# Optimization experiments

Hardware: AMD Instinct MI355X
Metric: run time of the kernel (lower is better)

Reference implementation:

```python
import jax, jax.numpy as jnp
import numpy as np

DIM = 1024
HEADS = 16
DIM_HEAD = 64
INNER = HEADS * DIM_HEAD
SCALE = DIM_HEAD ** -0.5


def setup_inputs() -> dict:
    key = jax.random.key(0)
    kx, kq, kk, kv, ko = jax.random.split(key, 5)
    B, N = 2, 2048
    s = DIM ** -0.5
    return {
        "x": jax.random.normal(kx, (B, N, DIM), dtype=jnp.float32),
        "Wq": jax.random.normal(kq, (DIM, INNER), dtype=jnp.float32) * s,
        "Wk": jax.random.normal(kk, (DIM, INNER), dtype=jnp.float32) * s,
        "Wv": jax.random.normal(kv, (DIM, INNER), dtype=jnp.float32) * s,
        "Wo": jax.random.normal(ko, (INNER, DIM), dtype=jnp.float32) * s,
    }


def reference(x, Wq, Wk, Wv, Wo):
    B, N, _ = x.shape
    # projections, split heads: b n (h d) -> b h n d
    def split(t):
        return t.reshape(B, N, HEADS, DIM_HEAD).transpose(0, 2, 1, 3)
    q = split(x @ Wq)
    k = split(x @ Wk)
    v = split(x @ Wv)
    # scores [B,H,N,N]
    dots = jnp.einsum("bhnd,bhmd->bhnm", q, k) * SCALE
    # causal mask: positions j > i masked
    causal = jnp.triu(jnp.ones((N, N), dtype=bool), k=1)
    dots = jnp.where(causal, -jnp.inf, dots)
    attn = jax.nn.softmax(dots, axis=-1)
    out = jnp.einsum("bhnm,bhmd->bhnd", attn, v)
    out = out.transpose(0, 2, 1, 3).reshape(B, N, INNER)
    return out @ Wo
```

## Files before the change

### kernel.cpp

```cpp
#include <hip/hip_runtime.h>

typedef unsigned short u16;
typedef unsigned int u32;
typedef __attribute__((ext_vector_type(8))) short short8;
typedef __attribute__((ext_vector_type(4))) short s16x4;
typedef __attribute__((ext_vector_type(4))) float f32x4;
typedef __attribute__((ext_vector_type(16))) float f32x16;
typedef __attribute__((ext_vector_type(4))) u32 u32x4;

typedef const __attribute__((address_space(1))) void* gptr_t;
typedef __attribute__((address_space(3))) void* sptr_t;

#define N_SEQ 2048
#define DIM 1024
#define INNER 1024
#define NTOK 4096
#define QKV_LD 3072

__device__ __forceinline__ u16 f2b(float f) {
  union { float f; unsigned u; } v; v.f = f;
  unsigned r = v.u + 0x7fffu + ((v.u >> 16) & 1u);
  return (u16)(r >> 16);
}

__global__ __launch_bounds__(256) void cast_x_kernel(const float* __restrict__ src,
                                                     u16* __restrict__ dst) {
  const size_t i = (size_t)blockIdx.x * 256 + threadIdx.x;
  const f32x4* s = (const f32x4*)(src + i * 8);
  f32x4 a = s[0], b = s[1];
  short8 o;
#pragma unroll
  for (int j = 0; j < 4; ++j) { o[j] = (short)f2b(a[j]); o[4 + j] = (short)f2b(b[j]); }
  *(short8*)(dst + i * 8) = o;
}

__global__ __launch_bounds__(256) void transpose_cast4_kernel(const float* __restrict__ Wq,
                                                              const float* __restrict__ Wk,
                                                              const float* __restrict__ Wv,
                                                              const float* __restrict__ Wo,
                                                              u16* __restrict__ wqkvt,
                                                              u16* __restrict__ wot) {
  const int z = blockIdx.z;
  const float* src = (z == 0) ? Wq : (z == 1) ? Wk : (z == 2) ? Wv : Wo;
  u16* dst = (z == 3) ? wot : wqkvt + (size_t)z * 1024 * 1024;
  __shared__ u16 tile[64][65];
  const int n0 = blockIdx.x * 64, k0 = blockIdx.y * 64;
  for (int i = threadIdx.x; i < 4096; i += 256) {
    const int r = i >> 6, c = i & 63;
    tile[r][c] = f2b(src[(size_t)(k0 + r) * 1024 + n0 + c]);
  }
  __syncthreads();
  for (int i = threadIdx.x; i < 4096; i += 256) {
    const int r = i >> 6, c = i & 63;
    dst[(size_t)(n0 + r) * 1024 + k0 + c] = tile[c][r];
  }
}

__global__ __launch_bounds__(256) void transpose_v_kernel(const u16* __restrict__ qkv,
                                                          u16* __restrict__ vt) {
  __shared__ u16 t[64][72];
  const int nt0 = blockIdx.x * 64;
  const int bh = blockIdx.y;
  const int b = bh >> 4, h = bh & 15;
  const u16* src = qkv + (size_t)b * N_SEQ * QKV_LD + 2048 + h * 64;
#pragma unroll
  for (int i = 0; i < 2; ++i) {
    const int cid = i * 256 + threadIdx.x;
    const int r = cid >> 3, c = (cid & 7) * 8;
    *(short8*)&t[r][c] = *(const short8*)(src + (size_t)(nt0 + r) * QKV_LD + c);
  }
  __syncthreads();
#pragma unroll
  for (int i = 0; i < 2; ++i) {
    const int cid = i * 256 + threadIdx.x;
    const int d = cid >> 3, c = (cid & 7) * 8;
    short8 v;
#pragma unroll
    for (int j = 0; j < 8; ++j) v[j] = t[c + j][d];
    *(short8*)(vt + ((size_t)bh * 64 + d) * N_SEQ + nt0 + c) = v;
  }
}

template <typename OutT>
__global__ __launch_bounds__(256) void gemm_tn(const u16* __restrict__ A,
                                               const u16* __restrict__ Bt,
                                               OutT* __restrict__ C,
                                               int M, int N, int K) {
  __shared__ u16 Al[128 * 64];
  __shared__ u16 Bl[128 * 64];
  const int tid = threadIdx.x;
  const int w = tid >> 6, lane = tid & 63;
  const int l15 = lane & 15, lg = lane >> 4;
  const int wr = w >> 1, wc = w & 1;
  const int nwg = gridDim.x * gridDim.y;
  int bid = blockIdx.y * gridDim.x + blockIdx.x;
  bid = (bid & 7) * (nwg >> 3) + (bid >> 3);
  const int bx = bid % gridDim.x, by = bid / gridDim.x;
  const int m0 = by * 128, n0 = bx * 128;

  f32x4 acc[4][4] = {};

  for (int k0 = 0; k0 < K; k0 += 64) {
#pragma unroll
    for (int i = 0; i < 4; ++i) {
      const int chunk = (w << 2) + i;
      const int e = (chunk << 9) + lane * 8;
      const int row = e >> 6, col = e & 63;
      const u16* ga = A + (size_t)(m0 + row) * K + k0 + col;
      __builtin_amdgcn_global_load_lds((gptr_t)ga, (sptr_t)(Al + (chunk << 9)), 16, 0, 0);
      const u16* gb = Bt + (size_t)(n0 + row) * K + k0 + col;
      __builtin_amdgcn_global_load_lds((gptr_t)gb, (sptr_t)(Bl + (chunk << 9)), 16, 0, 0);
    }
    __syncthreads();
#pragma unroll
    for (int kk = 0; kk < 2; ++kk) {
      short8 af[4], bf[4];
#pragma unroll
      for (int m = 0; m < 4; ++m)
        af[m] = *(const short8*)(Al + ((wr * 64 + m * 16 + l15) << 6) + kk * 32 + lg * 8);
#pragma unroll
      for (int n = 0; n < 4; ++n)
        bf[n] = *(const short8*)(Bl + ((wc * 64 + n * 16 + l15) << 6) + kk * 32 + lg * 8);
#pragma unroll
      for (int m = 0; m < 4; ++m)
#pragma unroll
        for (int n = 0; n < 4; ++n)
          acc[m][n] = __builtin_amdgcn_mfma_f32_16x16x32_bf16(af[m], bf[n], acc[m][n], 0, 0, 0);
    }
    __syncthreads();
  }

#pragma unroll
  for (int m = 0; m < 4; ++m)
#pragma unroll
    for (int n = 0; n < 4; ++n)
#pragma unroll
      for (int r = 0; r < 4; ++r) {
        const int row = m0 + wr * 64 + m * 16 + lg * 4 + r;
        const int col = n0 + wc * 64 + n * 16 + l15;
        const float v = acc[m][n][r];
        if constexpr (sizeof(OutT) == 2) C[(size_t)row * N + col] = (OutT)f2b(v);
        else                             C[(size_t)row * N + col] = (OutT)v;
      }
}

__global__ __launch_bounds__(64) void attn_kernel(const u16* __restrict__ qkv,
                                                  const u16* __restrict__ vt,
                                                  u16* __restrict__ attnb) {
  const int bx = blockIdx.x;
  const int bh = bx & 31;
  const int qw = 63 - (bx >> 5);
  const int b = bh >> 4, h = bh & 15;
  const int lane = threadIdx.x;
  const int l31 = lane & 31, hh = lane >> 5;
  const int qrow = qw * 32 + l31;

  __shared__ u16 Kl[64 * 64];
  __shared__ u16 Vl[64 * 64];

  const u16* base  = qkv + (size_t)b * N_SEQ * QKV_LD;
  const u16* kbase = base + 1024 + h * 64;
  const u16* vbase = vt + (size_t)bh * 64 * N_SEQ;

  short8 bq[4];
#pragma unroll
  for (int ks = 0; ks < 4; ++ks)
    bq[ks] = *(const short8*)(base + (size_t)qrow * QKV_LD + h * 64 + ks * 16 + hh * 8);

  f32x16 o0 = {}, o1 = {};
  float m_run = -3.0e38f, l_run = 0.f;
  const float kscale = 0.125f * 1.4426950408889634f;
  const int nt = (qw >> 1) + 1;

  for (int jt = 0; jt < nt; ++jt) {
    const int kvs = jt * 64;

#pragma unroll
    for (int i = 0; i < 8; ++i) {
      const int cid = i * 64 + lane;
      const int row = cid >> 3, cs = (cid & 7) ^ (row & 7);
      __builtin_amdgcn_global_load_lds(
          (gptr_t)(kbase + (size_t)(kvs + row) * QKV_LD + cs * 8),
          (sptr_t)(Kl + i * 512), 16, 0, 0);
      __builtin_amdgcn_global_load_lds(
          (gptr_t)(vbase + (size_t)row * N_SEQ + kvs + cs * 8),
          (sptr_t)(Vl + i * 512), 16, 0, 0);
    }
    asm volatile("s_waitcnt vmcnt(0)" ::: "memory");

    f32x16 p0 = {}, p1 = {};
    __builtin_amdgcn_s_setprio(1);
#pragma unroll
    for (int ks = 0; ks < 4; ++ks) {
      const int r0 = l31, r1 = 32 + l31;
      short8 ak0 = *(const short8*)(Kl + r0 * 64 + (((ks * 2 + hh) ^ (r0 & 7)) * 8));
      short8 ak1 = *(const short8*)(Kl + r1 * 64 + (((ks * 2 + hh) ^ (r1 & 7)) * 8));
      p0 = __builtin_amdgcn_mfma_f32_32x32x16_bf16(ak0, bq[ks], p0, 0, 0, 0);
      p1 = __builtin_amdgcn_mfma_f32_32x32x16_bf16(ak1, bq[ks], p1, 0, 0, 0);
    }
    __builtin_amdgcn_s_setprio(0);

    if (jt == nt - 1) {
      const int kvb = kvs + 4 * hh;
#pragma unroll
      for (int r = 0; r < 16; ++r) {
        const int off = (r & 3) + 8 * (r >> 2);
        if (kvb + off > qrow)      p0[r] = -3.0e38f;
        if (kvb + 32 + off > qrow) p1[r] = -3.0e38f;
      }
    }

    float mt = -3.0e38f;
#pragma unroll
    for (int r = 0; r < 16; ++r) { mt = fmaxf(mt, p0[r]); mt = fmaxf(mt, p1[r]); }
    mt = fmaxf(mt, __shfl_xor(mt, 32, 64));
    const float mn = fmaxf(m_run, mt);
    if (!__all(mn - m_run <= 44.f)) {
      const float sf = exp2f((m_run - mn) * kscale);
      m_run = mn;
      l_run *= sf;
      o0 *= sf; o1 *= sf;
    }
    float ps = 0.f;
#pragma unroll
    for (int r = 0; r < 16; ++r) {
      const float e0 = exp2f((p0[r] - m_run) * kscale);
      const float e1 = exp2f((p1[r] - m_run) * kscale);
      p0[r] = e0; p1[r] = e1;
      ps += e0 + e1;
    }
    ps += __shfl_xor(ps, 32, 64);
    l_run += ps;

    u32 bpw[4][4];
#define PACK_TILE(P, kf)                                                    \
    {                                                                       \
      _Pragma("unroll")                                                     \
      for (int a2 = 0; a2 < 2; ++a2) {                                      \
        _Pragma("unroll")                                                   \
        for (int c2 = 0; c2 < 2; ++c2) {                                    \
          u32 X, Y;                                                         \
          asm("v_cvt_pk_bf16_f32 %0, %1, %2" : "=v"(X)                      \
              : "v"(P[8 * a2 + 2 * c2]), "v"(P[8 * a2 + 2 * c2 + 1]));      \
          asm("v_cvt_pk_bf16_f32 %0, %1, %2" : "=v"(Y)                      \
              : "v"(P[8 * a2 + 4 + 2 * c2]), "v"(P[8 * a2 + 5 + 2 * c2]));  \
          asm("v_permlane32_swap_b32 %0, %1" : "+v"(X), "+v"(Y));           \
          bpw[(kf) * 2 + a2][c2] = X;                                       \
          bpw[(kf) * 2 + a2][2 + c2] = Y;                                   \
        }                                                                   \
      }                                                                     \
    }
    PACK_TILE(p0, 0)
    PACK_TILE(p1, 1)
#undef PACK_TILE

    __builtin_amdgcn_s_setprio(1);
#pragma unroll
    for (int ks16 = 0; ks16 < 4; ++ks16) {
      u32x4 t = {bpw[ks16][0], bpw[ks16][1], bpw[ks16][2], bpw[ks16][3]};
      short8 bp = __builtin_bit_cast(short8, t);
      const int cb = ks16 * 2 + hh;
      const int row0 = l31, row1 = 32 + l31;
      short8 av0 = *(const short8*)(Vl + row0 * 64 + ((cb ^ (row0 & 7)) * 8));
      short8 av1 = *(const short8*)(Vl + row1 * 64 + ((cb ^ (row1 & 7)) * 8));
      o0 = __builtin_amdgcn_mfma_f32_32x32x16_bf16(av0, bp, o0, 0, 0, 0);
      o1 = __builtin_amdgcn_mfma_f32_32x32x16_bf16(av1, bp, o1, 0, 0, 0);
    }
    __builtin_amdgcn_s_setprio(0);
  }

  const float inv = 1.f / l_run;
  u16* orow = attnb + ((size_t)b * N_SEQ + qrow) * INNER + h * 64 + 4 * hh;
#pragma unroll
  for (int rq = 0; rq < 4; ++rq) {
    s16x4 sv0, sv1;
#pragma unroll
    for (int j = 0; j < 4; ++j) {
      sv0[j] = (short)f2b(o0[rq * 4 + j] * inv);
      sv1[j] = (short)f2b(o1[rq * 4 + j] * inv);
    }
    *(s16x4*)(orow + rq * 8) = sv0;
    *(s16x4*)(orow + 32 + rq * 8) = sv1;
  }
}

extern "C" void kernel_launch(void* const* d_in, const int* in_sizes, int n_in,
                              void* d_out, int out_size, void* d_ws, size_t ws_size,
                              hipStream_t stream) {
  const float* x  = (const float*)d_in[0];
  const float* Wq = (const float*)d_in[1];
  const float* Wk = (const float*)d_in[2];
  const float* Wv = (const float*)d_in[3];
  const float* Wo = (const float*)d_in[4];
  float* out = (float*)d_out;

  u16* xb    = (u16*)d_ws;
  u16* wqkvt = xb    + (size_t)NTOK * DIM;
  u16* wot   = wqkvt + (size_t)3 * INNER * DIM;
  u16* qkv   = wot   + (size_t)DIM * INNER;
  u16* attnb = qkv   + (size_t)NTOK * QKV_LD;
  u16* vtb   = attnb + (size_t)NTOK * INNER;

  cast_x_kernel<<<dim3(NTOK * DIM / (256 * 8)), 256, 0, stream>>>(x, xb);
  transpose_cast4_kernel<<<dim3(16, 16, 4), 256, 0, stream>>>(Wq, Wk, Wv, Wo, wqkvt, wot);

  gemm_tn<u16><<<dim3(3072 / 128, 4096 / 128), 256, 0, stream>>>(xb, wqkvt, qkv, NTOK, 3072, DIM);
  transpose_v_kernel<<<dim3(32, 32), 256, 0, stream>>>(qkv, vtb);
  attn_kernel<<<dim3(2048), 64, 0, stream>>>(qkv, vtb, attnb);
  gemm_tn<float><<<dim3(1024 / 128, 4096 / 128), 256, 0, stream>>>(attnb, wot, out, NTOK, INNER, INNER);
}
```

Before: 160.4 us.

## Double-buffer K/V tiles in LDS and prioritize long-running attention waves

Splits the K/V LDS staging into two buffers so the next tile's global-to-LDS loads are issued before computing on the current tile, waiting only on the older batch of loads. Replaces per-MFMA-section priority toggling with a fixed high priority for waves handling the last query blocks, which have the most KV tiles. Also splits the softmax row-sum into four independent accumulators to shorten the dependency chain. This doubles LDS use per block, which could lower occupancy. Each wave reads only its own lanes' loads, so no barrier is needed with 64-thread blocks.

```diff
diff --git a/kernel.cpp b/kernel.cpp
--- a/kernel.cpp
+++ b/kernel.cpp
@@ -155,8 +155,10 @@
   const int l31 = lane & 31, hh = lane >> 5;
   const int qrow = qw * 32 + l31;
 
-  __shared__ u16 Kl[64 * 64];
-  __shared__ u16 Vl[64 * 64];
+  __shared__ u16 Kl[2][64 * 64];
+  __shared__ u16 Vl[2][64 * 64];
+
+  if (qw >= 48) __builtin_amdgcn_s_setprio(1);
 
   const u16* base  = qkv + (size_t)b * N_SEQ * QKV_LD;
   const u16* kbase = base + 1024 + h * 64;
@@ -172,33 +174,47 @@
   const float kscale = 0.125f * 1.4426950408889634f;
   const int nt = (qw >> 1) + 1;
 
+#define STAGE(jt_, bsel)                                                            \
+  {                                                                                 \
+    const int kvs_ = (jt_) * 64;                                                    \
+    u16* Klb_ = Kl[bsel];                                                           \
+    u16* Vlb_ = Vl[bsel];                                                           \
+    _Pragma("unroll")                                                               \
+    for (int i = 0; i < 8; ++i) {                                                   \
+      const int cid = i * 64 + lane;                                                \
+      const int row = cid >> 3, cs = (cid & 7) ^ (row & 7);                         \
+      __builtin_amdgcn_global_load_lds(                                             \
+          (gptr_t)(kbase + (size_t)(kvs_ + row) * QKV_LD + cs * 8),                 \
+          (sptr_t)(Klb_ + i * 512), 16, 0, 0);                                      \
+      __builtin_amdgcn_global_load_lds(                                             \
+          (gptr_t)(vbase + (size_t)row * N_SEQ + kvs_ + cs * 8),                    \
+          (sptr_t)(Vlb_ + i * 512), 16, 0, 0);                                      \
+    }                                                                               \
+  }
+
+  STAGE(0, 0)
+
   for (int jt = 0; jt < nt; ++jt) {
     const int kvs = jt * 64;
-
-#pragma unroll
-    for (int i = 0; i < 8; ++i) {
-      const int cid = i * 64 + lane;
-      const int row = cid >> 3, cs = (cid & 7) ^ (row & 7);
-      __builtin_amdgcn_global_load_lds(
-          (gptr_t)(kbase + (size_t)(kvs + row) * QKV_LD + cs * 8),
-          (sptr_t)(Kl + i * 512), 16, 0, 0);
-      __builtin_amdgcn_global_load_lds(
-          (gptr_t)(vbase + (size_t)row * N_SEQ + kvs + cs * 8),
-          (sptr_t)(Vl + i * 512), 16, 0, 0);
-    }
-    asm volatile("s_waitcnt vmcnt(0)" ::: "memory");
+    const int cur = jt & 1;
+    if (jt + 1 < nt) {
+      STAGE(jt + 1, cur ^ 1)
+      asm volatile("s_waitcnt vmcnt(16)" ::: "memory");
+    } else {
+      asm volatile("s_waitcnt vmcnt(0)" ::: "memory");
+    }
+    const u16* Klb = Kl[cur];
+    const u16* Vlb = Vl[cur];
 
     f32x16 p0 = {}, p1 = {};
-    __builtin_amdgcn_s_setprio(1);
 #pragma unroll
     for (int ks = 0; ks < 4; ++ks) {
       const int r0 = l31, r1 = 32 + l31;
-      short8 ak0 = *(const short8*)(Kl + r0 * 64 + (((ks * 2 + hh) ^ (r0 & 7)) * 8));
-      short8 ak1 = *(const short8*)(Kl + r1 * 64 + (((ks * 2 + hh) ^ (r1 & 7)) * 8));
+      short8 ak0 = *(const short8*)(Klb + r0 * 64 + (((ks * 2 + hh) ^ (r0 & 7)) * 8));
+      short8 ak1 = *(const short8*)(Klb + r1 * 64 + (((ks * 2 + hh) ^ (r1 & 7)) * 8));
       p0 = __builtin_amdgcn_mfma_f32_32x32x16_bf16(ak0, bq[ks], p0, 0, 0, 0);
       p1 = __builtin_amdgcn_mfma_f32_32x32x16_bf16(ak1, bq[ks], p1, 0, 0, 0);
     }
-    __builtin_amdgcn_s_setprio(0);
 
     if (jt == nt - 1) {
       const int kvb = kvs + 4 * hh;
@@ -221,14 +237,15 @@
       l_run *= sf;
       o0 *= sf; o1 *= sf;
     }
-    float ps = 0.f;
+    float psa = 0.f, psb = 0.f, psc = 0.f, psd = 0.f;
 #pragma unroll
     for (int r = 0; r < 16; ++r) {
       const float e0 = exp2f((p0[r] - m_run) * kscale);
       const float e1 = exp2f((p1[r] - m_run) * kscale);
       p0[r] = e0; p1[r] = e1;
-      ps += e0 + e1;
-    }
+      if (r & 1) { psb += e0; psd += e1; } else { psa += e0; psc += e1; }
+    }
+    float ps = (psa + psb) + (psc + psd);
     ps += __shfl_xor(ps, 32, 64);
     l_run += ps;
 
@@ -254,20 +271,19 @@
     PACK_TILE(p1, 1)
 #undef PACK_TILE
 
-    __builtin_amdgcn_s_setprio(1);
 #pragma unroll
     for (int ks16 = 0; ks16 < 4; ++ks16) {
       u32x4 t = {bpw[ks16][0], bpw[ks16][1], bpw[ks16][2], bpw[ks16][3]};
       short8 bp = __builtin_bit_cast(short8, t);
       const int cb = ks16 * 2 + hh;
       const int row0 = l31, row1 = 32 + l31;
-      short8 av0 = *(const short8*)(Vl + row0 * 64 + ((cb ^ (row0 & 7)) * 8));
-      short8 av1 = *(const short8*)(Vl + row1 * 64 + ((cb ^ (row1 & 7)) * 8));
+      short8 av0 = *(const short8*)(Vlb + row0 * 64 + ((cb ^ (row0 & 7)) * 8));
+      short8 av1 = *(const short8*)(Vlb + row1 * 64 + ((cb ^ (row1 & 7)) * 8));
       o0 = __builtin_amdgcn_mfma_f32_32x32x16_bf16(av0, bp, o0, 0, 0, 0);
       o1 = __builtin_amdgcn_mfma_f32_32x32x16_bf16(av1, bp, o1, 0, 0, 0);
     }
-    __builtin_amdgcn_s_setprio(0);
-  }
+  }
+#undef STAGE
 
   const float inv = 1.f / l_run;
   u16* orow = attnb + ((size_t)b * N_SEQ + qrow) * INNER + h * 64 + 4 * hh;
```

After: 169.7 us. 5.8% more time.
